# Performance work log

Measured on AMD Instinct MI355X. Metric: run time of the kernel, lower is better.

Reference implementation:

```python
import jax, jax.numpy as jnp
import numpy as np

VS = 0.05        # voxel_size
R_KEEP = 1.25    # radius keep padding
D_AN = 0.5       # d_an2an anchor z offset
G = 64           # fixed voxel grid per axis (covers the r_keep ball)
G3 = G ** 3
B, N = 4, 65536
C_F, H4, W4 = 32, 128, 128


def setup_inputs() -> dict:
    key = jax.random.key(0)
    ks = jax.random.split(key, 6)
    pelvis = jnp.tile(jnp.array([0.0, 0.0, 3.0], jnp.float32), (B, 1, 1).__class__((B, 1, 1))) if False else (
        jnp.broadcast_to(jnp.array([0.0, 0.0, 3.0], jnp.float32), (B, 1, 3))
        + 0.1 * jax.random.normal(ks[0], (B, 1, 3), jnp.float32))
    points = pelvis + 0.6 * jax.random.normal(ks[1], (B, N, 3), jnp.float32)
    fmap_img = jax.random.normal(ks[2], (B, C_F, H4, W4), jnp.float32)
    K = jnp.broadcast_to(jnp.array([[500.0, 0.0, 256.0], [0.0, 500.0, 256.0], [0.0, 0.0, 1.0]], jnp.float32), (B, 3, 3))
    bbx_lurb = jnp.broadcast_to(jnp.array([0.0, 0.0, 512.0, 512.0], jnp.float32), (B, 4))
    W1 = 0.1 * jax.random.normal(ks[3], (35, 64), jnp.float32)
    b1 = jnp.zeros((64,), jnp.float32)
    W2 = 0.1 * jax.random.normal(ks[4], (64, 12), jnp.float32)
    b2 = jnp.zeros((12,), jnp.float32)
    return {"points": points, "fmap_img": fmap_img, "pelvis": pelvis, "K": K,
            "bbx_lurb": bbx_lurb, "W1": W1, "b1": b1, "W2": W2, "b2": b2}


def _bilinear(fmap, u, v):
    # fmap [C,H,W]; u,v pixel coords [M]; align_corners=True, zeros padding
    H, W = fmap.shape[1], fmap.shape[2]
    x0 = jnp.floor(u); y0 = jnp.floor(v)
    wx = u - x0; wy = v - y0

    def fetch(xi, yi):
        inb = (xi >= 0) & (xi <= W - 1) & (yi >= 0) & (yi <= H - 1)
        xc = jnp.clip(xi, 0, W - 1).astype(jnp.int32)
        yc = jnp.clip(yi, 0, H - 1).astype(jnp.int32)
        return fmap[:, yc, xc] * inb[None].astype(fmap.dtype)  # [C,M]

    v00 = fetch(x0, y0); v10 = fetch(x0 + 1, y0)
    v01 = fetch(x0, y0 + 1); v11 = fetch(x0 + 1, y0 + 1)
    out = (v00 * (1 - wx) * (1 - wy) + v10 * wx * (1 - wy)
           + v01 * (1 - wx) * wy + v11 * wx * wy)
    return out.T  # [M,C]


def reference(points, fmap_img, pelvis, K, bbx_lurb, W1, b1, W2, b2):
    a_mid = pelvis[:, 0]                                   # [B,3] detached pelvis anchor
    dz = jnp.array([0.0, 0.0, D_AN], jnp.float32)
    anchors = jnp.stack([a_mid - dz, a_mid, a_mid + dz], 1)  # [B,3,3]

    # radius-based nearby point search (get_nearby_points, p=2)
    d = jnp.linalg.norm(points[:, :, None, :] - anchors[:, None, :, :], axis=-1)  # [B,N,3]
    nearby = jnp.min(d, axis=-1) <= R_KEEP                 # [B,N]
    nearby = jnp.where(nearby.any(-1, keepdims=True), nearby, True)  # empty fallback: all points

    # voxelize (initial_voxelize): unique floor(p/vs) cells inside fixed grid around mid anchor
    v = jnp.floor(points / VS).astype(jnp.int32)           # [B,N,3]
    v0 = jnp.floor(a_mid / VS).astype(jnp.int32) - G // 2  # [B,3]
    local = v - v0[:, None, :]
    inb = jnp.all((local >= 0) & (local < G), -1) & nearby
    flat = local[..., 0] * G * G + local[..., 1] * G + local[..., 2]
    flat = jnp.where(inb, flat, G3)
    occ = jax.vmap(lambda f: jax.ops.segment_sum(jnp.ones_like(f), f, num_segments=G3 + 1))(flat)[:, :G3] > 0  # [B,G3]

    # voxel centers x_ori_xyz = C*vs + vs/2
    gi = jnp.arange(G3)
    grid = jnp.stack([gi // (G * G), (gi // G) % G, gi % G], -1)      # [G3,3]
    centers = (v0[:, None, :] + grid[None]).astype(jnp.float32) * VS + VS / 2  # [B,G3,3]

    # project to image, normalize by bbox, grid_sample image features
    fx = K[:, 0, 0][:, None]; fy = K[:, 1, 1][:, None]
    cx = K[:, 0, 2][:, None]; cy = K[:, 1, 2][:, None]
    z = centers[..., 2]
    u = centers[..., 0] / z * fx + cx
    vpix = centers[..., 1] / z * fy + cy
    u01 = (u - bbx_lurb[:, None, 0]) / (bbx_lurb[:, None, 2] - bbx_lurb[:, None, 0])
    v01 = (vpix - bbx_lurb[:, None, 1]) / (bbx_lurb[:, None, 3] - bbx_lurb[:, None, 1])
    Wf, Hf = fmap_img.shape[3], fmap_img.shape[2]
    feat_img = jax.vmap(_bilinear)(fmap_img, u01 * (Wf - 1), v01 * (Hf - 1))  # [B,G3,32]

    # feat = [anchor_mid - vox_xyz, sampled feats]; contact_net (pointwise MLP stand-in for SPVCNN)
    feat = jnp.concatenate([a_mid[:, None] - centers, feat_img], -1)  # [B,G3,35]
    h = jax.nn.relu(feat @ W1 + b1)
    out = h @ W2 + b2                                       # [B,G3,12]

    # scatter-softmax aggregate over occupied voxels: softmax(sigmoid(conf)) weighted mean
    conf = out[..., 0]
    offset = out[..., 1:4]
    s = jnp.where(occ, jax.nn.sigmoid(conf), -1e9)
    w = jax.nn.softmax(s, axis=-1)                          # [B,G3]
    xyz = jnp.einsum('bg,bgc->bc', w, centers + offset)     # [B,3]
    refined = jnp.where(jnp.isnan(xyz).any(-1, keepdims=True), a_mid, xyz)
    return refined, out
```

## Files before the change

kernel.cpp:

```cpp
#include <hip/hip_runtime.h>
#include <math.h>

#define BB 4
#define NN 65536
#define G 64
#define G3 (G*G*G)
#define CF 32
#define HF 128
#define WF 128
#define VSc 0.05f
#define R2c 1.5625f

#define BANY_OFF (2*BB*G3)
#define PART_OFF (BANY_OFF + 1024)
#define PART2_OFF (PART_OFF + 4096*16)
#define FMT_OFF  (PART2_OFF + 4096*16)
#define FMT_SZ   (BB*HF*WF*CF*2)
#define W1P_OFF  (FMT_OFF + FMT_SZ)
#define W2P_OFF  (W1P_OFF + 8192)

typedef __attribute__((ext_vector_type(8))) short short8;
typedef __attribute__((ext_vector_type(4))) float floatx4;

__device__ __forceinline__ ushort f2bf(float x) {
    union { float f; unsigned u; } v; v.f = x;
    unsigned r = v.u + 0x7FFF + ((v.u >> 16) & 1);
    return (ushort)(r >> 16);
}

__device__ __forceinline__ unsigned cvt_pk_bf16(float lo, float hi) {
    unsigned r;
    asm("v_cvt_pk_bf16_f32 %0, %1, %2" : "=v"(r) : "v"(lo), "v"(hi));
    return r;
}

__global__ __launch_bounds__(256) void prep_kernel(const float* __restrict__ pts,
                                                   const float* __restrict__ pelvis,
                                                   const float* __restrict__ fmap,
                                                   unsigned char* __restrict__ occ2,
                                                   unsigned char* __restrict__ blockAny,
                                                   ushort* __restrict__ fmapT,
                                                   const float* __restrict__ W1,
                                                   const float* __restrict__ W2,
                                                   ushort* __restrict__ w1p,
                                                   ushort* __restrict__ w2p) {
    __shared__ float tile[CF][65];
    int bi = blockIdx.x;

    if (bi < (BB * NN) / 256) {
        int idx = bi * 256 + threadIdx.x;
        int b = idx >> 16;
        const float* p = pts + (size_t)idx * 3;
        float px = p[0], py = p[1], pz = p[2];
        float ax = pelvis[b * 3 + 0], ay = pelvis[b * 3 + 1], az = pelvis[b * 3 + 2];

        float dx = px - ax, dy = py - ay, dz = pz - az;
        float rxy = dx * dx + dy * dy;
        float d0 = dz * dz;
        float dm = (dz + 0.5f) * (dz + 0.5f);
        float dp = (dz - 0.5f) * (dz - 0.5f);
        float mind2 = rxy + fminf(d0, fminf(dm, dp));
        bool nearby = mind2 <= R2c;

        int vx = (int)floorf(px / VSc);
        int vy = (int)floorf(py / VSc);
        int vz = (int)floorf(pz / VSc);
        int v0x = (int)floorf(ax / VSc) - 32;
        int v0y = (int)floorf(ay / VSc) - 32;
        int v0z = (int)floorf(az / VSc) - 32;
        int lx = vx - v0x, ly = vy - v0y, lz = vz - v0z;
        bool inb = ((unsigned)lx < 64u) && ((unsigned)ly < 64u) && ((unsigned)lz < 64u);
        if (inb) {
            int flat = b * G3 + (lx << 12) + (ly << 6) + lz;
            if (nearby) {
                *(ushort*)(occ2 + 2 * (size_t)flat) = 0x0101;
            } else {
                occ2[2 * (size_t)flat] = 1;
            }
        }
        unsigned long long bal = __ballot(nearby);
        if ((threadIdx.x & 63) == 0 && bal != 0ULL) blockAny[bi] = 1;
        return;
    }

    if (bi == 2 * (BB * NN) / 256) {
        int t = threadIdx.x;
        for (int s = t; s < 512; s += 256) {
            int kt = s >> 8, nt = (s >> 6) & 3, quad = (s >> 4) & 3, n16 = s & 15;
            short8 w;
#pragma unroll
            for (int j = 0; j < 8; ++j) {
                int kk = kt * 32 + quad * 8 + j;
                int row = (kk < 32) ? (3 + kk) : (kk - 32);
                w[j] = (kk < 35) ? (short)f2bf(W1[row * 64 + nt * 16 + n16]) : (short)0;
            }
            *(short8*)(w1p + s * 8) = w;
        }
        if (t < 128) {
            int kt = t >> 6, quad = (t >> 4) & 3, n16 = t & 15;
            short8 w;
#pragma unroll
            for (int j = 0; j < 8; ++j) {
                int phys = kt * 32 + quad * 8 + j;
                int c = (phys & 3) * 16 + (phys >> 2);
                w[j] = (n16 < 12) ? (short)f2bf(W2[c * 12 + n16]) : (short)0;
            }
            *(short8*)(w2p + t * 8) = w;
        }
        return;
    }

    int tb = bi - (BB * NN) / 256;
    int xc = (tb & 1) * 64;
    int y  = (tb >> 1) & (HF - 1);
    int b  = tb >> 8;
    int t = threadIdx.x;
#pragma unroll
    for (int i = 0; i < 8; ++i) {
        int e = i * 256 + t;
        int c = e >> 6, p = e & 63;
        tile[c][p] = fmap[(((size_t)b * CF + c) * HF + y) * WF + xc + p];
    }
    __syncthreads();
    unsigned* dst32 = (unsigned*)fmapT;
#pragma unroll
    for (int i = 0; i < 4; ++i) {
        int e = i * 256 + t;
        int pix = e >> 4, cp = e & 15;
        unsigned val = cvt_pk_bf16(tile[cp * 2][pix], tile[cp * 2 + 1][pix]);
        dst32[((((size_t)b * HF + y) * WF + xc + pix) << 4) + cp] = val;
    }
}

__global__ __launch_bounds__(256, 4) void voxel_kernel(
    const ushort* __restrict__ fmapT, const float* __restrict__ pelvis,
    const float* __restrict__ Kmat, const float* __restrict__ bbx,
    const ushort* __restrict__ w1p, const ushort* __restrict__ w2p,
    const float* __restrict__ b1, const float* __restrict__ b2,
    const ushort* __restrict__ occ2,
    float4* __restrict__ partials, float4* __restrict__ partials2,
    float* __restrict__ outBig) {
    __shared__ __align__(16) char ldsRaw[4][9216];
    __shared__ float red[4][8];

    int blk = blockIdx.x;
    int b = blk >> 10;
    int wv = threadIdx.x >> 6, lane = threadIdx.x & 63;
    int quad = lane >> 4, n16 = lane & 15;
    int g = ((blk & 1023) << 8) + (wv << 6) + lane;
    ushort* A = (ushort*)ldsRaw[wv];

    ushort oc2 = occ2[(size_t)b * G3 + g];

    float ax = pelvis[b * 3 + 0], ay = pelvis[b * 3 + 1], az = pelvis[b * 3 + 2];
    float fx = Kmat[b * 9 + 0], fy = Kmat[b * 9 + 4];
    float cxp = Kmat[b * 9 + 2], cyp = Kmat[b * 9 + 5];
    float l = bbx[b * 4 + 0], t = bbx[b * 4 + 1];
    float r = bbx[b * 4 + 2], btm = bbx[b * 4 + 3];
    float inv_w = 1.0f / (r - l), inv_h = 1.0f / (btm - t);

    int v0x = (int)floorf(ax / VSc) - 32;
    int v0y = (int)floorf(ay / VSc) - 32;
    int v0z = (int)floorf(az / VSc) - 32;

    int gx = g >> 12, gy = (g >> 6) & 63, gz = g & 63;
    float cxx = (float)(v0x + gx) * VSc + 0.025f;
    float cyy = (float)(v0y + gy) * VSc + 0.025f;
    float czz = (float)(v0z + gz) * VSc + 0.025f;

    float z = czz;
    float u = cxx / z * fx + cxp;
    float vp = cyy / z * fy + cyp;
    float uu = (u - l) * inv_w * (float)(WF - 1);
    float vv = (vp - t) * inv_h * (float)(HF - 1);
    float x0f = floorf(uu), y0f = floorf(vv);
    float wx = uu - x0f, wy = vv - y0f;
    int x0 = (int)x0f, y0 = (int)y0f;
    int x1 = x0 + 1, y1 = y0 + 1;
    bool mx0 = (unsigned)x0 < (unsigned)WF;
    bool mx1 = (unsigned)x1 < (unsigned)WF;
    bool my0 = (unsigned)y0 < (unsigned)HF;
    bool my1 = (unsigned)y1 < (unsigned)HF;
    int xc0 = min(max(x0, 0), WF - 1), xc1 = min(max(x1, 0), WF - 1);
    int yc0 = min(max(y0, 0), HF - 1), yc1 = min(max(y1, 0), HF - 1);

    const ushort* fb = fmapT + (size_t)b * HF * WF * CF;
    const uint4* q00 = (const uint4*)(fb + (size_t)(yc0 * WF + xc0) * CF);
    const uint4* q10 = (const uint4*)(fb + (size_t)(yc0 * WF + xc1) * CF);
    const uint4* q01 = (const uint4*)(fb + (size_t)(yc1 * WF + xc0) * CF);
    const uint4* q11 = (const uint4*)(fb + (size_t)(yc1 * WF + xc1) * CF);
    unsigned r00[16], r10[16], r01[16], r11[16];
#pragma unroll
    for (int j = 0; j < 4; ++j) {
        *(uint4*)(r00 + 4 * j) = q00[j];
        *(uint4*)(r10 + 4 * j) = q10[j];
        *(uint4*)(r01 + 4 * j) = q01[j];
        *(uint4*)(r11 + 4 * j) = q11[j];
    }

    float w00 = (1.0f - wx) * (1.0f - wy) * ((mx0 && my0) ? 1.0f : 0.0f);
    float w10 = wx * (1.0f - wy) * ((mx1 && my0) ? 1.0f : 0.0f);
    float w01 = (1.0f - wx) * wy * ((mx0 && my1) ? 1.0f : 0.0f);
    float w11 = wx * wy * ((mx1 && my1) ? 1.0f : 0.0f);

    float feat[35];
    feat[32] = ax - cxx;
    feat[33] = ay - cyy;
    feat[34] = az - czz;
#pragma unroll
    for (int d = 0; d < 16; ++d) {
        float a00l = __uint_as_float(r00[d] << 16), a00h = __uint_as_float(r00[d] & 0xFFFF0000u);
        float a10l = __uint_as_float(r10[d] << 16), a10h = __uint_as_float(r10[d] & 0xFFFF0000u);
        float a01l = __uint_as_float(r01[d] << 16), a01h = __uint_as_float(r01[d] & 0xFFFF0000u);
        float a11l = __uint_as_float(r11[d] << 16), a11h = __uint_as_float(r11[d] & 0xFFFF0000u);
        feat[2 * d]     = fmaf(a11l, w11, fmaf(a01l, w01, fmaf(a10l, w10, a00l * w00)));
        feat[2 * d + 1] = fmaf(a11h, w11, fmaf(a01h, w01, fmaf(a10h, w10, a00h * w00)));
    }

#pragma unroll
    for (int i = 0; i < 4; ++i) {
        uint4 v;
        v.x = cvt_pk_bf16(feat[8 * i + 0], feat[8 * i + 1]);
        v.y = cvt_pk_bf16(feat[8 * i + 2], feat[8 * i + 3]);
        v.z = cvt_pk_bf16(feat[8 * i + 4], feat[8 * i + 5]);
        v.w = cvt_pk_bf16(feat[8 * i + 6], feat[8 * i + 7]);
        *(uint4*)(A + lane * 72 + i * 8) = v;
    }
    {
        uint4 v;
        v.x = cvt_pk_bf16(feat[32], feat[33]);
        v.y = cvt_pk_bf16(feat[34], 0.0f);
        v.z = 0; v.w = 0;
        *(uint4*)(A + lane * 72 + 32) = v;
        uint4 z4 = {0, 0, 0, 0};
        *(uint4*)(A + lane * 72 + 40) = z4;
        *(uint4*)(A + lane * 72 + 48) = z4;
        *(uint4*)(A + lane * 72 + 56) = z4;
    }

    const short8* W1v = (const short8*)w1p;
    const short8* W2v = (const short8*)w2p;
    short8 B1f[2][4];
#pragma unroll
    for (int kt = 0; kt < 2; ++kt)
#pragma unroll
        for (int nt = 0; nt < 4; ++nt)
            B1f[kt][nt] = W1v[((kt * 4 + nt) * 4 + quad) * 16 + n16];
    short8 B2f[2];
#pragma unroll
    for (int kt = 0; kt < 2; ++kt)
        B2f[kt] = W2v[(kt * 4 + quad) * 16 + n16];
    float b1v[4];
#pragma unroll
    for (int nt = 0; nt < 4; ++nt) b1v[nt] = b1[nt * 16 + n16];
    float b2v = (n16 < 12) ? b2[n16] : 0.0f;

    floatx4 c1[4][4];
#pragma unroll
    for (int mt = 0; mt < 4; ++mt)
#pragma unroll
        for (int nt = 0; nt < 4; ++nt) {
            floatx4 c = {b1v[nt], b1v[nt], b1v[nt], b1v[nt]};
            c1[mt][nt] = c;
        }
#pragma unroll
    for (int mt = 0; mt < 4; ++mt) {
        short8 a0 = *(short8*)(A + (mt * 16 + n16) * 72 + quad * 8);
        short8 a1 = *(short8*)(A + (mt * 16 + n16) * 72 + 32 + quad * 8);
#pragma unroll
        for (int nt = 0; nt < 4; ++nt) {
            c1[mt][nt] = __builtin_amdgcn_mfma_f32_16x16x32_bf16(a0, B1f[0][nt], c1[mt][nt], 0, 0, 0);
            c1[mt][nt] = __builtin_amdgcn_mfma_f32_16x16x32_bf16(a1, B1f[1][nt], c1[mt][nt], 0, 0, 0);
        }
    }

#pragma unroll
    for (int mt = 0; mt < 4; ++mt)
#pragma unroll
        for (int rr = 0; rr < 4; ++rr) {
            float h0 = fmaxf(c1[mt][0][rr], 0.0f);
            float h1 = fmaxf(c1[mt][1][rr], 0.0f);
            float h2 = fmaxf(c1[mt][2][rr], 0.0f);
            float h3 = fmaxf(c1[mt][3][rr], 0.0f);
            uint2 uv;
            uv.x = cvt_pk_bf16(h0, h1);
            uv.y = cvt_pk_bf16(h2, h3);
            *(uint2*)(A + (mt * 16 + quad * 4 + rr) * 72 + n16 * 4) = uv;
        }

    floatx4 c2[4];
#pragma unroll
    for (int mt = 0; mt < 4; ++mt) {
        floatx4 c = {b2v, b2v, b2v, b2v};
        c2[mt] = c;
    }
#pragma unroll
    for (int mt = 0; mt < 4; ++mt) {
        short8 a0 = *(short8*)(A + (mt * 16 + n16) * 72 + quad * 8);
        short8 a1 = *(short8*)(A + (mt * 16 + n16) * 72 + 32 + quad * 8);
        c2[mt] = __builtin_amdgcn_mfma_f32_16x16x32_bf16(a0, B2f[0], c2[mt], 0, 0, 0);
        c2[mt] = __builtin_amdgcn_mfma_f32_16x16x32_bf16(a1, B2f[1], c2[mt], 0, 0, 0);
    }

    float* O = (float*)ldsRaw[wv];
#pragma unroll
    for (int mt = 0; mt < 4; ++mt)
#pragma unroll
        for (int rr = 0; rr < 4; ++rr)
            O[(mt * 16 + quad * 4 + rr) * 20 + n16] = c2[mt][rr];

    floatx4 o0 = *(floatx4*)(O + lane * 20 + 0);
    floatx4 o1 = *(floatx4*)(O + lane * 20 + 4);
    floatx4 o2 = *(floatx4*)(O + lane * 20 + 8);

    floatx4* dst = (floatx4*)(outBig + (size_t)(b * G3 + g) * 12);
    __builtin_nontemporal_store(o0, dst + 0);
    __builtin_nontemporal_store(o1, dst + 1);
    __builtin_nontemporal_store(o2, dst + 2);

    float sig = 1.0f / (1.0f + __expf(-o0.x));
    float e = __expf(sig - 1.0f);
    float wxx = cxx + o0.y, wyy = cyy + o0.z, wzz = czz + o0.w;
    float eN = ((oc2 >> 8) != 0) ? e : 0.0f;
    float eI = ((oc2 & 0xFF) != 0) ? e : 0.0f;
    float sN0 = eN, sN1 = eN * wxx, sN2 = eN * wyy, sN3 = eN * wzz;
    float sI0 = eI, sI1 = eI * wxx, sI2 = eI * wyy, sI3 = eI * wzz;
#pragma unroll
    for (int off = 32; off > 0; off >>= 1) {
        sN0 += __shfl_down(sN0, off, 64);
        sN1 += __shfl_down(sN1, off, 64);
        sN2 += __shfl_down(sN2, off, 64);
        sN3 += __shfl_down(sN3, off, 64);
        sI0 += __shfl_down(sI0, off, 64);
        sI1 += __shfl_down(sI1, off, 64);
        sI2 += __shfl_down(sI2, off, 64);
        sI3 += __shfl_down(sI3, off, 64);
    }
    if ((threadIdx.x & 63) == 0) {
        red[wv][0] = sN0; red[wv][1] = sN1; red[wv][2] = sN2; red[wv][3] = sN3;
        red[wv][4] = sI0; red[wv][5] = sI1; red[wv][6] = sI2; red[wv][7] = sI3;
    }
    __syncthreads();
    if (threadIdx.x == 0) {
        float t0 = red[0][0] + red[1][0] + red[2][0] + red[3][0];
        float t1 = red[0][1] + red[1][1] + red[2][1] + red[3][1];
        float t2 = red[0][2] + red[1][2] + red[2][2] + red[3][2];
        float t3 = red[0][3] + red[1][3] + red[2][3] + red[3][3];
        partials[blk] = make_float4(t0, t1, t2, t3);
        float u0 = red[0][4] + red[1][4] + red[2][4] + red[3][4];
        float u1 = red[0][5] + red[1][5] + red[2][5] + red[3][5];
        float u2 = red[0][6] + red[1][6] + red[2][6] + red[3][6];
        float u3 = red[0][7] + red[1][7] + red[2][7] + red[3][7];
        partials2[blk] = make_float4(u0, u1, u2, u3);
    }
}

__global__ __launch_bounds__(256) void reduce_kernel(const float4* __restrict__ partials,
                                                     const float4* __restrict__ partials2,
                                                     const unsigned char* __restrict__ blockAny,
                                                     const float* __restrict__ pelvis,
                                                     float* __restrict__ out) {
    __shared__ float sh[4][256];
    __shared__ int anyFlag;
    int b = blockIdx.x, t = threadIdx.x;
    if (t == 0) anyFlag = 0;
    __syncthreads();
    if (blockAny[b * 256 + t]) anyFlag = 1;
    __syncthreads();
    const float4* P = anyFlag ? partials : partials2;

    float s0 = 0, s1 = 0, s2 = 0, s3 = 0;
#pragma unroll
    for (int i = 0; i < 4; ++i) {
        float4 p = P[b * 1024 + i * 256 + t];
        s0 += p.x; s1 += p.y; s2 += p.z; s3 += p.w;
    }
    sh[0][t] = s0; sh[1][t] = s1; sh[2][t] = s2; sh[3][t] = s3;
    __syncthreads();
    for (int st = 128; st > 0; st >>= 1) {
        if (t < st) {
            sh[0][t] += sh[0][t + st];
            sh[1][t] += sh[1][t + st];
            sh[2][t] += sh[2][t + st];
            sh[3][t] += sh[3][t + st];
        }
        __syncthreads();
    }
    if (t == 0) {
        float den = sh[0][0];
        float x = sh[1][0] / den;
        float y = sh[2][0] / den;
        float zz = sh[3][0] / den;
        bool bad = isnan(x) || isnan(y) || isnan(zz);
        out[b * 3 + 0] = bad ? pelvis[b * 3 + 0] : x;
        out[b * 3 + 1] = bad ? pelvis[b * 3 + 1] : y;
        out[b * 3 + 2] = bad ? pelvis[b * 3 + 2] : zz;
    }
}

extern "C" void kernel_launch(void* const* d_in, const int* in_sizes, int n_in,
                              void* d_out, int out_size, void* d_ws, size_t ws_size,
                              hipStream_t stream) {
    const float* points = (const float*)d_in[0];
    const float* fmap   = (const float*)d_in[1];
    const float* pelvis = (const float*)d_in[2];
    const float* Kmat   = (const float*)d_in[3];
    const float* bbx    = (const float*)d_in[4];
    const float* W1     = (const float*)d_in[5];
    const float* b1     = (const float*)d_in[6];
    const float* W2     = (const float*)d_in[7];
    const float* b2     = (const float*)d_in[8];
    float* out = (float*)d_out;

    char* ws = (char*)d_ws;
    unsigned char* occ2 = (unsigned char*)ws;
    unsigned char* bAny = (unsigned char*)(ws + BANY_OFF);
    float4* partials  = (float4*)(ws + PART_OFF);
    float4* partials2 = (float4*)(ws + PART2_OFF);
    ushort* fmapT   = (ushort*)(ws + FMT_OFF);
    ushort* w1p     = (ushort*)(ws + W1P_OFF);
    ushort* w2p     = (ushort*)(ws + W2P_OFF);

    hipMemsetAsync(ws, 0, BANY_OFF + 1024, stream);

    prep_kernel<<<2 * (BB * NN) / 256 + 1, 256, 0, stream>>>(points, pelvis, fmap,
                                                             occ2, bAny, fmapT,
                                                             W1, W2, w1p, w2p);
    voxel_kernel<<<(BB * G3) / 256, 256, 0, stream>>>(fmapT, pelvis, Kmat, bbx,
                                                      w1p, w2p, b1, b2,
                                                      (const ushort*)occ2,
                                                      partials, partials2, out + 12);
    reduce_kernel<<<BB, 256, 0, stream>>>(partials, partials2, bAny, pelvis, out);
}
```

Measured before the change: 137.5 us.

## Swizzle LDS activation tile, shrink LDS, coalesce output stores, raise occupancy

Replaces the padded 72-element row stride in the per-wave LDS tile with a 64-element row using an XOR swizzle on 16-byte units, so the LDS footprint drops and bank conflicts are still avoided. The reduction scratch is folded into spare space in the wave buffers, and launch bounds are raised to 5 blocks per CU to use the freed LDS and registers. Output stores are remapped so consecutive lanes write consecutive 16-byte chunks of the wave's contiguous output span, instead of each lane writing its own 48-byte row. The occupancy hint may force register spills, and the reduction scratch offset has to stay clear of the live output data.

```diff
diff --git a/kernel.cpp b/kernel.cpp
--- a/kernel.cpp
+++ b/kernel.cpp
@@ -33,6 +33,8 @@
     asm("v_cvt_pk_bf16_f32 %0, %1, %2" : "=v"(r) : "v"(lo), "v"(hi));
     return r;
 }
+
+#define AIDX(row, unit) (((row) << 6) + ((((unit) ^ ((row) & 7))) << 3))
 
 __global__ __launch_bounds__(256) void prep_kernel(const float* __restrict__ pts,
                                                    const float* __restrict__ pelvis,
@@ -132,7 +134,7 @@
     }
 }
 
-__global__ __launch_bounds__(256, 4) void voxel_kernel(
+__global__ __launch_bounds__(256, 5) void voxel_kernel(
     const ushort* __restrict__ fmapT, const float* __restrict__ pelvis,
     const float* __restrict__ Kmat, const float* __restrict__ bbx,
     const ushort* __restrict__ w1p, const ushort* __restrict__ w2p,
@@ -140,8 +142,7 @@
     const ushort* __restrict__ occ2,
     float4* __restrict__ partials, float4* __restrict__ partials2,
     float* __restrict__ outBig) {
-    __shared__ __align__(16) char ldsRaw[4][9216];
-    __shared__ float red[4][8];
+    __shared__ __align__(16) char ldsRaw[4][8192];
 
     int blk = blockIdx.x;
     int b = blk >> 10;
@@ -224,18 +225,18 @@
         v.y = cvt_pk_bf16(feat[8 * i + 2], feat[8 * i + 3]);
         v.z = cvt_pk_bf16(feat[8 * i + 4], feat[8 * i + 5]);
         v.w = cvt_pk_bf16(feat[8 * i + 6], feat[8 * i + 7]);
-        *(uint4*)(A + lane * 72 + i * 8) = v;
+        *(uint4*)(A + AIDX(lane, i)) = v;
     }
     {
         uint4 v;
         v.x = cvt_pk_bf16(feat[32], feat[33]);
         v.y = cvt_pk_bf16(feat[34], 0.0f);
         v.z = 0; v.w = 0;
-        *(uint4*)(A + lane * 72 + 32) = v;
+        *(uint4*)(A + AIDX(lane, 4)) = v;
         uint4 z4 = {0, 0, 0, 0};
-        *(uint4*)(A + lane * 72 + 40) = z4;
-        *(uint4*)(A + lane * 72 + 48) = z4;
-        *(uint4*)(A + lane * 72 + 56) = z4;
+        *(uint4*)(A + AIDX(lane, 5)) = z4;
+        *(uint4*)(A + AIDX(lane, 6)) = z4;
+        *(uint4*)(A + AIDX(lane, 7)) = z4;
     }
 
     const short8* W1v = (const short8*)w1p;
@@ -265,8 +266,9 @@
         }
 #pragma unroll
     for (int mt = 0; mt < 4; ++mt) {
-        short8 a0 = *(short8*)(A + (mt * 16 + n16) * 72 + quad * 8);
-        short8 a1 = *(short8*)(A + (mt * 16 + n16) * 72 + 32 + quad * 8);
+        int row = mt * 16 + n16;
+        short8 a0 = *(short8*)(A + AIDX(row, quad));
+        short8 a1 = *(short8*)(A + AIDX(row, 4 + quad));
 #pragma unroll
         for (int nt = 0; nt < 4; ++nt) {
             c1[mt][nt] = __builtin_amdgcn_mfma_f32_16x16x32_bf16(a0, B1f[0][nt], c1[mt][nt], 0, 0, 0);
@@ -285,7 +287,9 @@
             uint2 uv;
             uv.x = cvt_pk_bf16(h0, h1);
             uv.y = cvt_pk_bf16(h2, h3);
-            *(uint2*)(A + (mt * 16 + quad * 4 + rr) * 72 + n16 * 4) = uv;
+            int row = mt * 16 + quad * 4 + rr;
+            int addr = (row << 6) + ((((n16 >> 1) ^ (row & 7))) << 3) + ((n16 & 1) << 2);
+            *(uint2*)(A + addr) = uv;
         }
 
     floatx4 c2[4];
@@ -296,8 +300,9 @@
     }
 #pragma unroll
     for (int mt = 0; mt < 4; ++mt) {
-        short8 a0 = *(short8*)(A + (mt * 16 + n16) * 72 + quad * 8);
-        short8 a1 = *(short8*)(A + (mt * 16 + n16) * 72 + 32 + quad * 8);
+        int row = mt * 16 + n16;
+        short8 a0 = *(short8*)(A + AIDX(row, quad));
+        short8 a1 = *(short8*)(A + AIDX(row, 4 + quad));
         c2[mt] = __builtin_amdgcn_mfma_f32_16x16x32_bf16(a0, B2f[0], c2[mt], 0, 0, 0);
         c2[mt] = __builtin_amdgcn_mfma_f32_16x16x32_bf16(a1, B2f[1], c2[mt], 0, 0, 0);
     }
@@ -309,14 +314,17 @@
         for (int rr = 0; rr < 4; ++rr)
             O[(mt * 16 + quad * 4 + rr) * 20 + n16] = c2[mt][rr];
 
-    floatx4 o0 = *(floatx4*)(O + lane * 20 + 0);
-    floatx4 o1 = *(floatx4*)(O + lane * 20 + 4);
-    floatx4 o2 = *(floatx4*)(O + lane * 20 + 8);
-
-    floatx4* dst = (floatx4*)(outBig + (size_t)(b * G3 + g) * 12);
-    __builtin_nontemporal_store(o0, dst + 0);
-    __builtin_nontemporal_store(o1, dst + 1);
-    __builtin_nontemporal_store(o2, dst + 2);
+    size_t base = (size_t)(b * G3 + ((blk & 1023) << 8) + (wv << 6)) * 12;
+#pragma unroll
+    for (int j = 0; j < 3; ++j) {
+        int k = 4 * lane + 256 * j;
+        int vx12 = k / 12;
+        int c12 = k - vx12 * 12;
+        floatx4 val = *(floatx4*)(O + vx12 * 20 + c12);
+        __builtin_nontemporal_store(val, (floatx4*)(outBig + base + k));
+    }
+
+    floatx4 o0 = *(floatx4*)(O + lane * 20);
 
     float sig = 1.0f / (1.0f + __expf(-o0.x));
     float e = __expf(sig - 1.0f);
@@ -336,21 +344,21 @@
         sI2 += __shfl_down(sI2, off, 64);
         sI3 += __shfl_down(sI3, off, 64);
     }
+    float* redw = (float*)(ldsRaw[wv] + 5632);
     if ((threadIdx.x & 63) == 0) {
-        red[wv][0] = sN0; red[wv][1] = sN1; red[wv][2] = sN2; red[wv][3] = sN3;
-        red[wv][4] = sI0; red[wv][5] = sI1; red[wv][6] = sI2; red[wv][7] = sI3;
+        redw[0] = sN0; redw[1] = sN1; redw[2] = sN2; redw[3] = sN3;
+        redw[4] = sI0; redw[5] = sI1; redw[6] = sI2; redw[7] = sI3;
     }
     __syncthreads();
     if (threadIdx.x == 0) {
-        float t0 = red[0][0] + red[1][0] + red[2][0] + red[3][0];
-        float t1 = red[0][1] + red[1][1] + red[2][1] + red[3][1];
-        float t2 = red[0][2] + red[1][2] + red[2][2] + red[3][2];
-        float t3 = red[0][3] + red[1][3] + red[2][3] + red[3][3];
+        float t0 = 0, t1 = 0, t2 = 0, t3 = 0, u0 = 0, u1 = 0, u2 = 0, u3 = 0;
+#pragma unroll
+        for (int w = 0; w < 4; ++w) {
+            float* rw = (float*)(ldsRaw[w] + 5632);
+            t0 += rw[0]; t1 += rw[1]; t2 += rw[2]; t3 += rw[3];
+            u0 += rw[4]; u1 += rw[5]; u2 += rw[6]; u3 += rw[7];
+        }
         partials[blk] = make_float4(t0, t1, t2, t3);
-        float u0 = red[0][4] + red[1][4] + red[2][4] + red[3][4];
-        float u1 = red[0][5] + red[1][5] + red[2][5] + red[3][5];
-        float u2 = red[0][6] + red[1][6] + red[2][6] + red[3][6];
-        float u3 = red[0][7] + red[1][7] + red[2][7] + red[3][7];
         partials2[blk] = make_float4(u0, u1, u2, u3);
     }
 }
```

New measurement: 157.4 us. +14.4%, slower.
